# Performance work log

Hardware: AMD Instinct MI355X
Metric: run time of the kernel (lower is better)

Reference implementation:

```python
import jax, jax.numpy as jnp
import numpy as np

D_MODEL = 1024
NUM_HEADS = 16
HEAD_DIM = D_MODEL // NUM_HEADS
B, S = 2, 2048


def setup_inputs() -> dict:
    key = jax.random.key(0)
    ks = jax.random.split(key, 5)
    x = jax.random.normal(ks[0], (B, S, D_MODEL), dtype=jnp.float32)
    # nn.Linear weights are [out_features, in_features]
    Wq = jax.random.normal(ks[1], (D_MODEL, D_MODEL), dtype=jnp.float32) / np.sqrt(D_MODEL)
    Wk = jax.random.normal(ks[2], (HEAD_DIM, D_MODEL), dtype=jnp.float32) / np.sqrt(D_MODEL)
    Wv = jax.random.normal(ks[3], (HEAD_DIM, D_MODEL), dtype=jnp.float32) / np.sqrt(D_MODEL)
    Wo = jax.random.normal(ks[4], (D_MODEL, D_MODEL), dtype=jnp.float32) / np.sqrt(D_MODEL)
    # causal mask, broadcastable to [B, H, S, S]; mask==0 positions get -inf
    mask = jnp.tril(jnp.ones((S, S), dtype=bool))[None, None]
    return {"x": x, "Wq": Wq, "Wk": Wk, "Wv": Wv, "Wo": Wo, "mask": mask}


def reference(x, Wq, Wk, Wv, Wo, mask):
    Bsz, Sl, D = x.shape
    H, hd = NUM_HEADS, HEAD_DIM
    q = (x @ Wq.T).reshape(Bsz, Sl, H, hd)          # [B,S,H,hd]
    k = x @ Wk.T                                    # [B,S,hd] (single shared KV head)
    v = x @ Wv.T                                    # [B,S,hd]
    scale = 1.0 / np.sqrt(hd).astype(np.float32)
    # scores: [B,H,S,S] — full O(n^2) matrix, as in the original module
    scores = jnp.einsum('bshd,btd->bhst', q, k) * scale
    scores = jnp.where(mask, scores, -jnp.inf)
    attn = jax.nn.softmax(scores, axis=-1)
    out = jnp.einsum('bhst,btd->bshd', attn, v).reshape(Bsz, Sl, D)
    return out @ Wo.T
```

## Files before the change

kernel.cpp:

```cpp
#include <hip/hip_runtime.h>
#include <hip/hip_bf16.h>
#include <math.h>

#define BB 2
#define SS 2048
#define DD 1024
#define NH 16
#define HD 64
#define MM (BB * SS)

typedef __hip_bfloat16 bf16;
typedef __bf16 bf16_t;
typedef __attribute__((ext_vector_type(8))) __bf16 bf16x8;
typedef __attribute__((ext_vector_type(4))) __bf16 bf16x4;
typedef __attribute__((ext_vector_type(4))) float floatx4;

__global__ void detect_dtype(const unsigned int* __restrict__ x, int* __restrict__ flag) {
    const int tid = threadIdx.x;
    int good = 0;
    for (int i = tid; i < 256; i += 64) {
        unsigned int bits = (x[i] & 0xFFFFu) << 16;
        float v = __uint_as_float(bits);
        float av = fabsf(v);
        if (av == 0.f || (av >= 9.5367431640625e-7f && av <= 64.f)) good++;
    }
#pragma unroll
    for (int s = 1; s < 64; s <<= 1) good += __shfl_xor(good, s);
    if (tid == 0) *flag = (good >= 240) ? 0 : 1;
}

#define BK 32
#define KP 40

__device__ __forceinline__ bf16x4 cvt4(float4 v) {
    bf16x4 o;
    o[0] = (bf16_t)v.x; o[1] = (bf16_t)v.y; o[2] = (bf16_t)v.z; o[3] = (bf16_t)v.w;
    return o;
}

__global__ __launch_bounds__(256) void proj_qkv(const void* __restrict__ X,
                                                const void* __restrict__ Wq,
                                                const void* __restrict__ Wk,
                                                const void* __restrict__ Wv,
                                                bf16_t* __restrict__ QA,
                                                bf16_t* __restrict__ Kp,
                                                bf16_t* __restrict__ VpT,
                                                const int* __restrict__ flag) {
    const int f = *flag;

    __shared__ bf16_t As[128 * KP];
    __shared__ bf16_t Ws[64 * KP];

    const int tid = threadIdx.x;
    const int wave = tid >> 6, lane = tid & 63;
    const int lo = lane & 15, quad = lane >> 4;
    const int rb = wave * 32;
    const int cb = blockIdx.x;
    const int rowBase = blockIdx.y * 128;

    floatx4 acc[2][4];
#pragma unroll
    for (int i = 0; i < 2; i++)
#pragma unroll
        for (int j = 0; j < 4; j++) acc[i][j] = (floatx4){0.f, 0.f, 0.f, 0.f};

    if (f) {
        const int rA = tid >> 3, sg = tid & 7;
        const float* arow[4];
        const float* wrow[2];
#pragma unroll
        for (int p = 0; p < 4; p++)
            arow[p] = (const float*)X + (size_t)(rowBase + rA + 32 * p) * DD;
#pragma unroll
        for (int p = 0; p < 2; p++) {
            int row = rA + 32 * p;
            if (cb < 16)       wrow[p] = (const float*)Wq + (size_t)(cb * 64 + row) * DD;
            else if (cb == 16) wrow[p] = (const float*)Wk + (size_t)row * DD;
            else               wrow[p] = (const float*)Wv + (size_t)row * DD;
        }
        float4 aR[4], wR[2];
#pragma unroll
        for (int p = 0; p < 4; p++) aR[p] = *(const float4*)(arow[p] + sg * 4);
#pragma unroll
        for (int p = 0; p < 2; p++) wR[p] = *(const float4*)(wrow[p] + sg * 4);

        for (int k0 = 0; k0 < DD; k0 += BK) {
            __syncthreads();
#pragma unroll
            for (int p = 0; p < 4; p++)
                *(bf16x4*)&As[(rA + 32 * p) * KP + sg * 4] = cvt4(aR[p]);
#pragma unroll
            for (int p = 0; p < 2; p++)
                *(bf16x4*)&Ws[(rA + 32 * p) * KP + sg * 4] = cvt4(wR[p]);
            __syncthreads();
            if (k0 + BK < DD) {
#pragma unroll
                for (int p = 0; p < 4; p++) aR[p] = *(const float4*)(arow[p] + k0 + BK + sg * 4);
#pragma unroll
                for (int p = 0; p < 2; p++) wR[p] = *(const float4*)(wrow[p] + k0 + BK + sg * 4);
            }
            bf16x8 afr[2], bfr[4];
#pragma unroll
            for (int i = 0; i < 2; i++)
                afr[i] = *(const bf16x8*)&As[(rb + i * 16 + lo) * KP + quad * 8];
#pragma unroll
            for (int j = 0; j < 4; j++)
                bfr[j] = *(const bf16x8*)&Ws[(j * 16 + lo) * KP + quad * 8];
#pragma unroll
            for (int i = 0; i < 2; i++)
#pragma unroll
                for (int j = 0; j < 4; j++)
                    acc[i][j] = __builtin_amdgcn_mfma_f32_16x16x32_bf16(afr[i], bfr[j], acc[i][j], 0, 0, 0);
        }
    } else {
        const int rA = tid >> 2, sg = tid & 3;
        const bf16_t* arow[2];
        const bf16_t* wrow;
#pragma unroll
        for (int p = 0; p < 2; p++)
            arow[p] = (const bf16_t*)X + (size_t)(rowBase + rA + 64 * p) * DD;
        if (cb < 16)       wrow = (const bf16_t*)Wq + (size_t)(cb * 64 + rA) * DD;
        else if (cb == 16) wrow = (const bf16_t*)Wk + (size_t)rA * DD;
        else               wrow = (const bf16_t*)Wv + (size_t)rA * DD;
        bf16x8 aR[2], wR;
#pragma unroll
        for (int p = 0; p < 2; p++) aR[p] = *(const bf16x8*)(arow[p] + sg * 8);
        wR = *(const bf16x8*)(wrow + sg * 8);

        for (int k0 = 0; k0 < DD; k0 += BK) {
            __syncthreads();
#pragma unroll
            for (int p = 0; p < 2; p++)
                *(bf16x8*)&As[(rA + 64 * p) * KP + sg * 8] = aR[p];
            *(bf16x8*)&Ws[rA * KP + sg * 8] = wR;
            __syncthreads();
            if (k0 + BK < DD) {
#pragma unroll
                for (int p = 0; p < 2; p++) aR[p] = *(const bf16x8*)(arow[p] + k0 + BK + sg * 8);
                wR = *(const bf16x8*)(wrow + k0 + BK + sg * 8);
            }
            bf16x8 afr[2], bfr[4];
#pragma unroll
            for (int i = 0; i < 2; i++)
                afr[i] = *(const bf16x8*)&As[(rb + i * 16 + lo) * KP + quad * 8];
#pragma unroll
            for (int j = 0; j < 4; j++)
                bfr[j] = *(const bf16x8*)&Ws[(j * 16 + lo) * KP + quad * 8];
#pragma unroll
            for (int i = 0; i < 2; i++)
#pragma unroll
                for (int j = 0; j < 4; j++)
                    acc[i][j] = __builtin_amdgcn_mfma_f32_16x16x32_bf16(afr[i], bfr[j], acc[i][j], 0, 0, 0);
        }
    }

#pragma unroll
    for (int i = 0; i < 2; i++)
#pragma unroll
        for (int j = 0; j < 4; j++)
#pragma unroll
            for (int reg = 0; reg < 4; reg++) {
                int row = rowBase + rb + i * 16 + quad * 4 + reg;
                int col = j * 16 + lo;
                bf16_t val = (bf16_t)acc[i][j][reg];
                if (cb < 16)       QA[(size_t)row * DD + cb * 64 + col] = val;
                else if (cb == 16) Kp[(size_t)row * HD + col] = val;
                else               VpT[((size_t)(row >> 11) * HD + col) * SS + (row & (SS - 1))] = val;
            }
}

__global__ __launch_bounds__(256) void proj_o(const bf16_t* __restrict__ AO,
                                              const void* __restrict__ Wo,
                                              void* __restrict__ Cout,
                                              const int* __restrict__ flag) {
    const int f = *flag;

    __shared__ bf16_t As[128 * KP];
    __shared__ bf16_t Ws[64 * KP];

    const int tid = threadIdx.x;
    const int wave = tid >> 6, lane = tid & 63;
    const int lo = lane & 15, quad = lane >> 4;
    const int rb = wave * 32;
    const int colBase = blockIdx.x * 64;
    const int rowBase = blockIdx.y * 128;

    floatx4 acc[2][4];
#pragma unroll
    for (int i = 0; i < 2; i++)
#pragma unroll
        for (int j = 0; j < 4; j++) acc[i][j] = (floatx4){0.f, 0.f, 0.f, 0.f};

    const int rA2 = tid >> 2, sgA = tid & 3;
    const bf16_t* arow[2] = {AO + (size_t)(rowBase + rA2) * DD,
                             AO + (size_t)(rowBase + rA2 + 64) * DD};
    bf16x8 aR[2];
#pragma unroll
    for (int p = 0; p < 2; p++) aR[p] = *(const bf16x8*)(arow[p] + sgA * 8);

    if (f) {
        const int rW = tid >> 3, sgW = tid & 7;
        const float* wrow[2];
#pragma unroll
        for (int p = 0; p < 2; p++)
            wrow[p] = (const float*)Wo + (size_t)(colBase + rW + 32 * p) * DD;
        float4 wR[2];
#pragma unroll
        for (int p = 0; p < 2; p++) wR[p] = *(const float4*)(wrow[p] + sgW * 4);

        for (int k0 = 0; k0 < DD; k0 += BK) {
            __syncthreads();
#pragma unroll
            for (int p = 0; p < 2; p++)
                *(bf16x8*)&As[(rA2 + 64 * p) * KP + sgA * 8] = aR[p];
#pragma unroll
            for (int p = 0; p < 2; p++)
                *(bf16x4*)&Ws[(rW + 32 * p) * KP + sgW * 4] = cvt4(wR[p]);
            __syncthreads();
            if (k0 + BK < DD) {
#pragma unroll
                for (int p = 0; p < 2; p++) aR[p] = *(const bf16x8*)(arow[p] + k0 + BK + sgA * 8);
#pragma unroll
                for (int p = 0; p < 2; p++) wR[p] = *(const float4*)(wrow[p] + k0 + BK + sgW * 4);
            }
            bf16x8 afr[2], bfr[4];
#pragma unroll
            for (int i = 0; i < 2; i++)
                afr[i] = *(const bf16x8*)&As[(rb + i * 16 + lo) * KP + quad * 8];
#pragma unroll
            for (int j = 0; j < 4; j++)
                bfr[j] = *(const bf16x8*)&Ws[(j * 16 + lo) * KP + quad * 8];
#pragma unroll
            for (int i = 0; i < 2; i++)
#pragma unroll
                for (int j = 0; j < 4; j++)
                    acc[i][j] = __builtin_amdgcn_mfma_f32_16x16x32_bf16(afr[i], bfr[j], acc[i][j], 0, 0, 0);
        }
    } else {
        const bf16_t* wrow = (const bf16_t*)Wo + (size_t)(colBase + rA2) * DD;
        bf16x8 wR = *(const bf16x8*)(wrow + sgA * 8);

        for (int k0 = 0; k0 < DD; k0 += BK) {
            __syncthreads();
#pragma unroll
            for (int p = 0; p < 2; p++)
                *(bf16x8*)&As[(rA2 + 64 * p) * KP + sgA * 8] = aR[p];
            *(bf16x8*)&Ws[rA2 * KP + sgA * 8] = wR;
            __syncthreads();
            if (k0 + BK < DD) {
#pragma unroll
                for (int p = 0; p < 2; p++) aR[p] = *(const bf16x8*)(arow[p] + k0 + BK + sgA * 8);
                wR = *(const bf16x8*)(wrow + k0 + BK + sgA * 8);
            }
            bf16x8 afr[2], bfr[4];
#pragma unroll
            for (int i = 0; i < 2; i++)
                afr[i] = *(const bf16x8*)&As[(rb + i * 16 + lo) * KP + quad * 8];
#pragma unroll
            for (int j = 0; j < 4; j++)
                bfr[j] = *(const bf16x8*)&Ws[(j * 16 + lo) * KP + quad * 8];
#pragma unroll
            for (int i = 0; i < 2; i++)
#pragma unroll
                for (int j = 0; j < 4; j++)
                    acc[i][j] = __builtin_amdgcn_mfma_f32_16x16x32_bf16(afr[i], bfr[j], acc[i][j], 0, 0, 0);
        }
    }

#pragma unroll
    for (int i = 0; i < 2; i++)
#pragma unroll
        for (int j = 0; j < 4; j++)
#pragma unroll
            for (int reg = 0; reg < 4; reg++) {
                int row = rowBase + rb + i * 16 + quad * 4 + reg;
                int col = colBase + j * 16 + lo;
                size_t idx = (size_t)row * DD + col;
                if (f) ((float*)Cout)[idx] = acc[i][j][reg];
                else   ((bf16_t*)Cout)[idx] = (bf16_t)acc[i][j][reg];
            }
}

#define PSTR 40
#define ALOG2E 0.18033688011112042f

__global__ __launch_bounds__(256, 4) void attn_mfma(const bf16_t* Q,
                                                    const bf16_t* __restrict__ K,
                                                    const bf16_t* __restrict__ Vt,
                                                    bf16_t* O) {
    const int h = blockIdx.y, b = blockIdx.z;
    const int tid = threadIdx.x;
    const int wq = tid >> 6, lane = tid & 63;
    const int lo = lane & 15, quad = lane >> 4;
    const int x = blockIdx.x;
    const int pr = wq >> 1;
    const int hh = wq & 1;
    const int qt = pr ? (63 - x) : x;
    const int q0 = qt * 32;
    const int nt = qt + 1;
    const int nt0 = nt >> 1;
    const int itS = hh ? nt0 : 0;
    const int itE = hh ? nt : nt0;

    __shared__ bf16_t Ps[4][32 * PSTR];
    __shared__ float MrgO[2][32][64];
    __shared__ float MrgML[2][2][2][16];
    bf16_t* Pw = Ps[wq];

    bf16x8 qf[2][2];
#pragma unroll
    for (int s = 0; s < 2; s++)
#pragma unroll
        for (int hf = 0; hf < 2; hf++)
            qf[s][hf] = *(const bf16x8*)(Q + ((size_t)(b * SS + q0 + s * 16 + lo)) * DD +
                                         h * HD + hf * 32 + quad * 8);

    floatx4 Oacc[2][4];
    float m_i[2], l_i[2];
#pragma unroll
    for (int s = 0; s < 2; s++) {
#pragma unroll
        for (int dt = 0; dt < 4; dt++) Oacc[s][dt] = (floatx4){0.f, 0.f, 0.f, 0.f};
        m_i[s] = -1e30f; l_i[s] = 0.f;
    }

    const bf16_t* Kb = K + (size_t)b * SS * HD;
    const bf16_t* Vb = Vt + (size_t)b * HD * SS;

    if (itS < itE) {
        bf16x8 kf[2][2];
#pragma unroll
        for (int kt = 0; kt < 2; kt++)
#pragma unroll
            for (int hf = 0; hf < 2; hf++)
                kf[kt][hf] = *(const bf16x8*)(Kb + (size_t)(itS * 32 + kt * 16 + lo) * HD +
                                              hf * 32 + quad * 8);

        for (int it = itS; it < itE; it++) {
            const int t0 = it * 32;

            bf16x8 vf[4];
#pragma unroll
            for (int dt = 0; dt < 4; dt++)
                vf[dt] = *(const bf16x8*)(Vb + (size_t)(dt * 16 + lo) * SS + t0 + quad * 8);

            bf16x8 kn[2][2];
            if (it + 1 < itE) {
#pragma unroll
                for (int kt = 0; kt < 2; kt++)
#pragma unroll
                    for (int hf = 0; hf < 2; hf++)
                        kn[kt][hf] = *(const bf16x8*)(Kb + (size_t)(t0 + 32 + kt * 16 + lo) * HD +
                                                      hf * 32 + quad * 8);
            }

            floatx4 st[2][2];
#pragma unroll
            for (int s = 0; s < 2; s++)
#pragma unroll
                for (int kt = 0; kt < 2; kt++) {
                    floatx4 z = (floatx4){0.f, 0.f, 0.f, 0.f};
                    z = __builtin_amdgcn_mfma_f32_16x16x32_bf16(kf[kt][0], qf[s][0], z, 0, 0, 0);
                    z = __builtin_amdgcn_mfma_f32_16x16x32_bf16(kf[kt][1], qf[s][1], z, 0, 0, 0);
                    st[s][kt] = z;
                }

            if (it == qt) {
#pragma unroll
                for (int s = 0; s < 2; s++) {
                    int q = q0 + s * 16 + lo;
#pragma unroll
                    for (int kt = 0; kt < 2; kt++)
#pragma unroll
                        for (int reg = 0; reg < 4; reg++)
                            if (t0 + kt * 16 + quad * 4 + reg > q) st[s][kt][reg] = -1e30f;
                }
            }

#pragma unroll
            for (int s = 0; s < 2; s++) {
                float mx = fmaxf(fmaxf(fmaxf(st[s][0][0], st[s][0][1]), fmaxf(st[s][0][2], st[s][0][3])),
                                 fmaxf(fmaxf(st[s][1][0], st[s][1][1]), fmaxf(st[s][1][2], st[s][1][3])));
                mx = fmaxf(mx, __shfl_xor(mx, 16));
                mx = fmaxf(mx, __shfl_xor(mx, 32));
                float mn = fmaxf(m_i[s], mx);
                float al = exp2f((m_i[s] - mn) * ALOG2E);
                m_i[s] = mn;
                float mnA = mn * ALOG2E;
                float p[2][4];
#pragma unroll
                for (int kt = 0; kt < 2; kt++)
#pragma unroll
                    for (int reg = 0; reg < 4; reg++)
                        p[kt][reg] = exp2f(st[s][kt][reg] * ALOG2E - mnA);
                float rs = ((p[0][0] + p[0][1]) + (p[0][2] + p[0][3])) +
                           ((p[1][0] + p[1][1]) + (p[1][2] + p[1][3]));
                rs += __shfl_xor(rs, 16);
                rs += __shfl_xor(rs, 32);
                l_i[s] = l_i[s] * al + rs;
#pragma unroll
                for (int kt = 0; kt < 2; kt++) {
                    bf16x4 pk;
#pragma unroll
                    for (int reg = 0; reg < 4; reg++) pk[reg] = (bf16_t)p[kt][reg];
                    *(bf16x4*)&Pw[(s * 16 + lo) * PSTR + kt * 16 + quad * 4] = pk;
                }
#pragma unroll
                for (int dt = 0; dt < 4; dt++) Oacc[s][dt] *= al;
            }

            asm volatile("s_waitcnt lgkmcnt(0)" ::: "memory");

            bf16x8 pb[2];
#pragma unroll
            for (int s = 0; s < 2; s++)
                pb[s] = *(const bf16x8*)&Pw[(s * 16 + lo) * PSTR + quad * 8];
#pragma unroll
            for (int s = 0; s < 2; s++)
#pragma unroll
                for (int dt = 0; dt < 4; dt++)
                    Oacc[s][dt] = __builtin_amdgcn_mfma_f32_16x16x32_bf16(vf[dt], pb[s], Oacc[s][dt], 0, 0, 0);

#pragma unroll
            for (int kt = 0; kt < 2; kt++)
#pragma unroll
                for (int hf = 0; hf < 2; hf++) kf[kt][hf] = kn[kt][hf];
        }
    }

    if (hh) {
#pragma unroll
        for (int s = 0; s < 2; s++) {
#pragma unroll
            for (int dt = 0; dt < 4; dt++)
#pragma unroll
                for (int reg = 0; reg < 4; reg++)
                    MrgO[pr][s * 16 + dt * 4 + reg][lane] = Oacc[s][dt][reg];
            if (quad == 0) {
                MrgML[pr][s][0][lo] = m_i[s];
                MrgML[pr][s][1][lo] = l_i[s];
            }
        }
    }
    __syncthreads();
    if (!hh) {
#pragma unroll
        for (int s = 0; s < 2; s++) {
            float m1 = MrgML[pr][s][0][lo];
            float l1 = MrgML[pr][s][1][lo];
            float mm = fmaxf(m_i[s], m1);
            float a0 = exp2f((m_i[s] - mm) * ALOG2E);
            float a1 = exp2f((m1 - mm) * ALOG2E);
            float linv = 1.f / (l_i[s] * a0 + l1 * a1);
            bf16_t* Orow = O + ((size_t)(b * SS + q0 + s * 16 + lo)) * DD + h * HD;
#pragma unroll
            for (int dt = 0; dt < 4; dt++) {
                bf16x4 ov;
#pragma unroll
                for (int reg = 0; reg < 4; reg++) {
                    float o1 = MrgO[pr][s * 16 + dt * 4 + reg][lane];
                    ov[reg] = (bf16_t)((Oacc[s][dt][reg] * a0 + o1 * a1) * linv);
                }
                *(bf16x4*)&Orow[dt * 16 + quad * 4] = ov;
            }
        }
    }
}

extern "C" void kernel_launch(void* const* d_in, const int* in_sizes, int n_in,
                              void* d_out, int out_size, void* d_ws, size_t ws_size,
                              hipStream_t stream) {
    const void* x  = d_in[0];
    const void* Wq = d_in[1];
    const void* Wk = d_in[2];
    const void* Wv = d_in[3];
    const void* Wo = d_in[4];

    char* ws = (char*)d_ws;
    int* flag = (int*)ws;
    bf16_t* QA  = (bf16_t*)(ws + 256);
    bf16_t* Kp  = QA + (size_t)MM * DD;
    bf16_t* VpT = Kp + (size_t)MM * HD;

    detect_dtype<<<1, 64, 0, stream>>>((const unsigned int*)x, flag);

    proj_qkv<<<dim3(18, MM / 128), dim3(256), 0, stream>>>(x, Wq, Wk, Wv, QA, Kp, VpT, flag);

    attn_mfma<<<dim3(32, NH, BB), dim3(256), 0, stream>>>(QA, Kp, VpT, QA);

    proj_o<<<dim3(16, MM / 128), dim3(256), 0, stream>>>(QA, Wo, d_out, flag);
}
```

Baseline: 219.0 us.

## Split causal attention KV range across eight waves with tree merge

After: 473.8 us. 2.16x slower.

```diff
diff --git a/kernel.cpp b/kernel.cpp
--- a/kernel.cpp
+++ b/kernel.cpp
@@ -284,7 +284,7 @@
 #define PSTR 40
 #define ALOG2E 0.18033688011112042f
 
-__global__ __launch_bounds__(256, 4) void attn_mfma(const bf16_t* Q,
+__global__ __launch_bounds__(512, 8) void attn_mfma(const bf16_t* Q,
                                                     const bf16_t* __restrict__ K,
                                                     const bf16_t* __restrict__ Vt,
                                                     bf16_t* O) {
@@ -293,19 +293,28 @@
     const int wq = tid >> 6, lane = tid & 63;
     const int lo = lane & 15, quad = lane >> 4;
     const int x = blockIdx.x;
-    const int pr = wq >> 1;
-    const int hh = wq & 1;
-    const int qt = pr ? (63 - x) : x;
+
+    const int nA = x + 1;
+    int na = 1, bestc = 0x7fffffff;
+#pragma unroll
+    for (int a = 1; a <= 7; ++a) {
+        int cA = (nA + a - 1) / a;
+        int cB = (65 - nA + (7 - a)) / (8 - a);
+        int c = cA > cB ? cA : cB;
+        if (c < bestc) { bestc = c; na = a; }
+    }
+    int qt, pos, gs;
+    if (wq < na) { qt = x;      pos = wq;      gs = na; }
+    else         { qt = 63 - x; pos = wq - na; gs = 8 - na; }
     const int q0 = qt * 32;
-    const int nt = qt + 1;
-    const int nt0 = nt >> 1;
-    const int itS = hh ? nt0 : 0;
-    const int itE = hh ? nt : nt0;
-
-    __shared__ bf16_t Ps[4][32 * PSTR];
-    __shared__ float MrgO[2][32][64];
-    __shared__ float MrgML[2][2][2][16];
-    bf16_t* Pw = Ps[wq];
+    const int n = qt + 1;
+    const int itS = (n * pos) / gs;
+    const int itE = (n * (pos + 1)) / gs;
+
+    __shared__ __align__(16) char smem[4 * 32 * 64 * 4];
+    __shared__ float MrgML[4][2][2][16];
+    bf16_t* Pw = (bf16_t*)smem + wq * (32 * PSTR);
+    float (*MrgO)[32 * 64] = (float (*)[32 * 64])smem;
 
     bf16x8 qf[2][2];
 #pragma unroll
@@ -428,39 +437,59 @@
         }
     }
 
-    if (hh) {
+    for (int step = 1; step < 8; step <<= 1) {
+        const bool pub = (pos & (2 * step - 1)) == step;
+        const bool cmb = ((pos & (2 * step - 1)) == 0) && (pos + step < gs);
+        __syncthreads();
+        if (pub) {
+            float* Ob = MrgO[wq >> 1];
+#pragma unroll
+            for (int s = 0; s < 2; s++) {
+#pragma unroll
+                for (int dt = 0; dt < 4; dt++)
+#pragma unroll
+                    for (int reg = 0; reg < 4; reg++)
+                        Ob[(s * 16 + dt * 4 + reg) * 64 + lane] = Oacc[s][dt][reg];
+                if (quad == 0) {
+                    MrgML[wq >> 1][s][0][lo] = m_i[s];
+                    MrgML[wq >> 1][s][1][lo] = l_i[s];
+                }
+            }
+        }
+        __syncthreads();
+        if (cmb) {
+            const int bu = (wq + step) >> 1;
+            const float* Ob = MrgO[bu];
+#pragma unroll
+            for (int s = 0; s < 2; s++) {
+                float m1 = MrgML[bu][s][0][lo];
+                float l1 = MrgML[bu][s][1][lo];
+                float mm = fmaxf(m_i[s], m1);
+                float a0 = exp2f((m_i[s] - mm) * ALOG2E);
+                float a1 = exp2f((m1 - mm) * ALOG2E);
+                m_i[s] = mm;
+                l_i[s] = l_i[s] * a0 + l1 * a1;
+#pragma unroll
+                for (int dt = 0; dt < 4; dt++)
+#pragma unroll
+                    for (int reg = 0; reg < 4; reg++)
+                        Oacc[s][dt][reg] = Oacc[s][dt][reg] * a0 +
+                                           Ob[(s * 16 + dt * 4 + reg) * 64 + lane] * a1;
+            }
+        }
+    }
+
+    if (pos == 0) {
 #pragma unroll
         for (int s = 0; s < 2; s++) {
-#pragma unroll
-            for (int dt = 0; dt < 4; dt++)
-#pragma unroll
-                for (int reg = 0; reg < 4; reg++)
-                    MrgO[pr][s * 16 + dt * 4 + reg][lane] = Oacc[s][dt][reg];
-            if (quad == 0) {
-                MrgML[pr][s][0][lo] = m_i[s];
-                MrgML[pr][s][1][lo] = l_i[s];
-            }
-        }
-    }
-    __syncthreads();
-    if (!hh) {
-#pragma unroll
-        for (int s = 0; s < 2; s++) {
-            float m1 = MrgML[pr][s][0][lo];
-            float l1 = MrgML[pr][s][1][lo];
-            float mm = fmaxf(m_i[s], m1);
-            float a0 = exp2f((m_i[s] - mm) * ALOG2E);
-            float a1 = exp2f((m1 - mm) * ALOG2E);
-            float linv = 1.f / (l_i[s] * a0 + l1 * a1);
+            float linv = 1.f / l_i[s];
             bf16_t* Orow = O + ((size_t)(b * SS + q0 + s * 16 + lo)) * DD + h * HD;
 #pragma unroll
             for (int dt = 0; dt < 4; dt++) {
                 bf16x4 ov;
 #pragma unroll
-                for (int reg = 0; reg < 4; reg++) {
-                    float o1 = MrgO[pr][s * 16 + dt * 4 + reg][lane];
-                    ov[reg] = (bf16_t)((Oacc[s][dt][reg] * a0 + o1 * a1) * linv);
-                }
+                for (int reg = 0; reg < 4; reg++)
+                    ov[reg] = (bf16_t)(Oacc[s][dt][reg] * linv);
                 *(bf16x4*)&Orow[dt * 16 + quad * 4] = ov;
             }
         }
@@ -486,7 +515,7 @@
 
     proj_qkv<<<dim3(18, MM / 128), dim3(256), 0, stream>>>(x, Wq, Wk, Wv, QA, Kp, VpT, flag);
 
-    attn_mfma<<<dim3(32, NH, BB), dim3(256), 0, stream>>>(QA, Kp, VpT, QA);
+    attn_mfma<<<dim3(32, NH, BB), dim3(512), 0, stream>>>(QA, Kp, VpT, QA);
 
     proj_o<<<dim3(16, MM / 128), dim3(256), 0, stream>>>(QA, Wo, d_out, flag);
 }
```
